# Performance work log

Hardware: AMD Instinct MI355X
Metric: run time of the kernel (lower is better)

The kernel has to match this reference:

```python
import jax, jax.numpy as jnp
import numpy as np

NUM_EXPERTS = 8
HIDDEN = 1024
INTER = 1024
BATCH = 2
SEQ = 1024
TOP_K = 2
SWIGLU_ALPHA = 1.702
LIMIT = 7.0


def setup_inputs() -> dict:
    key = jax.random.key(0)
    ks = jax.random.split(key, 7)
    hidden_states = jax.random.normal(ks[0], (BATCH, SEQ, HIDDEN), jnp.float32)
    router_indices = jax.random.randint(ks[1], (BATCH * SEQ, TOP_K), 0, NUM_EXPERTS)
    routing_weights = jax.nn.softmax(
        jax.random.normal(ks[2], (BATCH * SEQ, NUM_EXPERTS), jnp.float32), axis=-1)
    scale = 0.02
    gate_up_proj = jax.random.normal(ks[3], (NUM_EXPERTS, HIDDEN, 2 * INTER), jnp.float32) * scale
    gate_up_proj_bias = jax.random.normal(ks[4], (NUM_EXPERTS, 2 * INTER), jnp.float32) * scale
    down_proj = jax.random.normal(ks[5], (NUM_EXPERTS, INTER, HIDDEN), jnp.float32) * scale
    down_proj_bias = jax.random.normal(ks[6], (NUM_EXPERTS, HIDDEN), jnp.float32) * scale
    return {
        "hidden_states": hidden_states,
        "router_indices": router_indices,
        "routing_weights": routing_weights,
        "gate_up_proj": gate_up_proj,
        "gate_up_proj_bias": gate_up_proj_bias,
        "down_proj": down_proj,
        "down_proj_bias": down_proj_bias,
    }


def _grouped_mm(x, w, expert_ids):
    """Grouped GEMM: y[t] = x[t] @ w[expert_ids[t]].

    x: [T, K], w: [E, K, N], expert_ids: [T] int.
    Reference form via one-hot masking (exact equivalent of torch._grouped_mm
    on expert-sorted tokens); guaranteed jit- and grad-safe.
    """
    onehot = jax.nn.one_hot(expert_ids, w.shape[0], dtype=x.dtype)  # [T, E]
    y_all = jnp.einsum('tk,ekn->etn', x, w)                         # [E, T, N]
    return jnp.einsum('te,etn->tn', onehot, y_all)                  # [T, N]


def _gpt_oss_swiglu(x):
    gate = jnp.minimum(x[..., ::2], LIMIT)
    up = jnp.clip(x[..., 1::2], -LIMIT, LIMIT)
    glu = gate * jax.nn.sigmoid(gate * SWIGLU_ALPHA)
    return (up + 1.0) * glu


def reference(hidden_states, router_indices, routing_weights,
              gate_up_proj, gate_up_proj_bias, down_proj, down_proj_bias):
    B = hidden_states.shape[0]
    H = hidden_states.shape[-1]
    x = hidden_states.reshape(-1, H)                       # [M, H]
    M = x.shape[0]
    top_k = router_indices.shape[1]
    num_experts = gate_up_proj.shape[0]

    # routing_weights is [M, num_experts] -> gather the top-k weights
    topk_weights = jnp.take_along_axis(routing_weights, router_indices, axis=1)  # [M, K]

    flat_experts = router_indices.reshape(-1)              # [T = M*K]
    sort_idx = jnp.argsort(flat_experts)                   # expert-sorted order
    sorted_pos = sort_idx // top_k                         # token id per slot
    expert_sorted = flat_experts[sort_idx]                 # [T]
    grouped = x[sorted_pos]                                # [T, H]

    gate_up = _grouped_mm(grouped, gate_up_proj, expert_sorted)
    gate_up = gate_up + gate_up_proj_bias[expert_sorted]   # per-expert bias
    inter = _gpt_oss_swiglu(gate_up)                       # [T, I]

    down = _grouped_mm(inter, down_proj, expert_sorted)
    down = down + down_proj_bias[expert_sorted]            # [T, H]
    down = down * topk_weights.reshape(-1)[sort_idx][:, None]

    out = jnp.zeros((M, H), x.dtype).at[sorted_pos].add(down)  # scatter-add combine
    return out.reshape(B, -1, H)
```

## Files before the change

### kernel.cpp

```cpp
#include <hip/hip_runtime.h>

#define NE 8
#define NH 1024
#define NI 1024
#define NGU 2048
#define MTOK 2048
#define TSLOT 4096

#define MAXT64 80
#define MAXT128 40

typedef short s16x8 __attribute__((ext_vector_type(8)));
typedef float f32x4 __attribute__((ext_vector_type(4)));
typedef unsigned short u16;

#define WS_SEG      0
#define WS_DESC64   64
#define WS_DESC128  384
#define WS_SLOT     1024
#define WS_POS      17408
#define WS_INTER    33792
#define WS_AREG     8422400UL
#define WS_WREG     12616704UL
#define WS_WTD      46171136UL
#define WS_NEED_FAST  46171136UL
#define WS_NEED_PIGGY 62948352UL

__device__ inline u16 f2bf(float f) {
    unsigned u = __builtin_bit_cast(unsigned, f);
    u += 0x7fffu + ((u >> 16) & 1u);
    return (u16)(u >> 16);
}

__device__ inline void lds_dma16(const u16* g, u16* l) {
    __builtin_amdgcn_global_load_lds(
        (const __attribute__((address_space(1))) unsigned int*)g,
        (__attribute__((address_space(3))) unsigned int*)l, 16, 0, 0);
}

__device__ inline int lds_off(int row, int blk) {
    return (row << 7) | (((blk ^ (row & 7)) & 7) << 4);
}

#define PIPE_FENCE asm volatile("" ::: "memory")
#define WAIT_VM6   asm volatile("s_waitcnt vmcnt(6)" ::: "memory")
#define WAIT_VM0   asm volatile("s_waitcnt vmcnt(0)" ::: "memory")

__device__ inline void tr_tile(const float* __restrict__ in, u16* __restrict__ outw,
                               int K, int N, int n0, int k0, int tid, u16 (*T)[66]) {
#pragma unroll
    for (int p = 0; p < 2; ++p) {
        int kr = p * 32 + (tid >> 4) * 2;
        int nc = (tid & 15) * 4;
        const float* r0 = in + (size_t)(k0 + kr) * N + n0 + nc;
        float4 v0 = *(const float4*)r0;
        float4 v1 = *(const float4*)(r0 + N);
#pragma unroll
        for (int i = 0; i < 4; ++i) {
            unsigned lo = f2bf(((const float*)&v0)[i]);
            unsigned hi = f2bf(((const float*)&v1)[i]);
            *(unsigned*)&T[nc + i][kr] = lo | (hi << 16);
        }
    }
    __syncthreads();
#pragma unroll
    for (int p = 0; p < 2; ++p) {
        int idx = p * 256 + tid;
        int nr = idx >> 3, kc = (idx & 7) * 8;
        unsigned q0 = *(const unsigned*)&T[nr][kc + 0];
        unsigned q1 = *(const unsigned*)&T[nr][kc + 2];
        unsigned q2 = *(const unsigned*)&T[nr][kc + 4];
        unsigned q3 = *(const unsigned*)&T[nr][kc + 6];
        uint4 vv = {q0, q1, q2, q3};
        *(uint4*)(outw + (size_t)(n0 + nr) * K + k0 + kc) = vv;
    }
}

__global__ __launch_bounds__(256) void k_tr(const float* __restrict__ W,
                                            u16* __restrict__ WT, int K, int N) {
    __shared__ u16 T[64][66];
    tr_tile(W + (size_t)blockIdx.z * K * N, WT + (size_t)blockIdx.z * N * K,
            K, N, blockIdx.x * 64, blockIdx.y * 64, threadIdx.x, T);
}

__global__ __launch_bounds__(256) void k_prep(
        const float* __restrict__ x, const int* __restrict__ ridx,
        const float* __restrict__ wgu,
        int* __restrict__ seg, int* __restrict__ d64, int* __restrict__ d128,
        int* __restrict__ slot_of, int* __restrict__ pos_of,
        u16* __restrict__ A, u16* __restrict__ wt_gu, float* __restrict__ out) {
    __shared__ int cnt[NE];
    __shared__ int cur[NE];
    __shared__ u16 T[64][66];
    int b = blockIdx.x;
    int tid = threadIdx.x;

    if (b == 0) {
        if (tid < NE) cnt[tid] = 0;
        __syncthreads();
        for (int s = tid; s < TSLOT; s += blockDim.x) atomicAdd(&cnt[ridx[s] & 7], 1);
        __syncthreads();
        if (tid == 0) {
            int a = 0;
            for (int e = 0; e < NE; ++e) { seg[e] = a; cur[e] = a; a += cnt[e]; }
            seg[NE] = a;
            int nt = 0;
            for (int e = 0; e < NE; ++e)
                for (int m0 = 0; m0 < cnt[e]; m0 += 64) d64[nt++] = (e << 16) | (m0 / 64);
            for (; nt < MAXT64; ++nt) d64[nt] = -1;
            nt = 0;
            for (int e = 0; e < NE; ++e)
                for (int m0 = 0; m0 < cnt[e]; m0 += 128) d128[nt++] = (e << 16) | (m0 / 128);
            for (; nt < MAXT128; ++nt) d128[nt] = -1;
        }
        __syncthreads();
        for (int s = tid; s < TSLOT; s += blockDim.x) {
            int e = ridx[s] & 7;
            int p = atomicAdd(&cur[e], 1);
            slot_of[p] = s;
            pos_of[s] = p;
        }
    } else if (b <= MTOK) {
        int t = b - 1;
        float4 v = ((const float4*)(x + (size_t)t * NH))[tid];
        ushort4 o;
        o.x = f2bf(v.x); o.y = f2bf(v.y); o.z = f2bf(v.z); o.w = f2bf(v.w);
        ((ushort4*)(A + (size_t)t * NH))[tid] = o;
        float4 z = {0.f, 0.f, 0.f, 0.f};
        ((float4*)(out + (size_t)t * NH))[tid] = z;
    } else {
        int id = b - (MTOK + 1);
        int e = id >> 9, rem = id & 511;
        int kblk = rem >> 5, nblk = rem & 31;
        tr_tile(wgu + (size_t)e * NH * NGU, wt_gu + (size_t)e * NGU * NH,
                NH, NGU, nblk * 64, kblk * 64, tid, T);
    }
}

__global__ __launch_bounds__(256) void k_gateup_f(
        const u16* __restrict__ A,
        const u16* __restrict__ wt,
        const float* __restrict__ bias,
        const int* __restrict__ seg, const int* __restrict__ desc,
        const int* __restrict__ slot_of,
        u16* __restrict__ inter,
        const float* __restrict__ wd,
        u16* __restrict__ wtd) {
    __shared__ __align__(16) char SM[49152];
    int tid = threadIdx.x;

    if (blockIdx.x >= MAXT128) {
        int id = (blockIdx.x - MAXT128) * 32 + blockIdx.y;
        int e = id >> 8, rem = id & 255;
        int kblk = rem >> 4, nblk = rem & 15;
        u16 (*T)[66] = (u16(*)[66])SM;
        tr_tile(wd + (size_t)e * NI * NH, wtd + (size_t)e * NH * NI,
                NI, NH, nblk * 64, kblk * 64, tid, T);
        return;
    }

    int d = desc[blockIdx.x];
    if (d < 0) return;
    int e = d >> 16, mt = d & 0xffff;
    int seg0 = seg[e], Te = seg[e + 1] - seg0, m0 = mt * 128;

    u16* As0 = (u16*)SM;
    u16* As1 = (u16*)(SM + 16384);
    u16* Bs0 = (u16*)(SM + 32768);
    u16* Bs1 = (u16*)(SM + 40960);

    int lane = tid & 63, w = tid >> 6;
    int ml = lane & 15, kq = lane >> 4;
    int wm = w >> 1, wn = w & 1;
    int n0 = blockIdx.y * 64;
    const u16* wte = wt + (size_t)e * NGU * NH;
    int dr = lane >> 3, db = (lane & 7) ^ dr;

    const u16* aptr[4];
#pragma unroll
    for (int c = 0; c < 4; ++c) {
        int gr = seg0 + m0 + c * 32 + w * 8 + dr;
        if (gr > TSLOT - 1) gr = TSLOT - 1;
        int tok = slot_of[gr] >> 1;
        aptr[c] = A + (size_t)tok * NH + db * 8;
    }
    const u16* bptr[2];
#pragma unroll
    for (int c = 0; c < 2; ++c)
        bptr[c] = wte + (size_t)(n0 + c * 32 + w * 8 + dr) * NH + db * 8;

    auto stage = [&](u16* AS, u16* BS, int kb) {
#pragma unroll
        for (int c = 0; c < 4; ++c) lds_dma16(aptr[c] + kb, AS + c * 2048 + w * 512);
#pragma unroll
        for (int c = 0; c < 2; ++c) lds_dma16(bptr[c] + kb, BS + c * 2048 + w * 512);
    };

    f32x4 zero = {0.f, 0.f, 0.f, 0.f};
    f32x4 acc[4][2];
#pragma unroll
    for (int i = 0; i < 4; ++i) { acc[i][0] = zero; acc[i][1] = zero; }

    auto compute = [&](const u16* AS, const u16* BS) {
#pragma unroll
        for (int kk = 0; kk < 64; kk += 32) {
            s16x8 af[4], bf[2];
#pragma unroll
            for (int i = 0; i < 4; ++i)
                af[i] = *(const s16x8*)((const char*)AS + lds_off(wm * 64 + i * 16 + ml, (kk >> 3) + kq));
#pragma unroll
            for (int i = 0; i < 2; ++i)
                bf[i] = *(const s16x8*)((const char*)BS + lds_off(wn * 32 + i * 16 + ml, (kk >> 3) + kq));
#pragma unroll
            for (int mi = 0; mi < 4; ++mi)
#pragma unroll
                for (int ni = 0; ni < 2; ++ni)
                    acc[mi][ni] = __builtin_amdgcn_mfma_f32_16x16x32_bf16(
                        af[mi], bf[ni], acc[mi][ni], 0, 0, 0);
        }
    };

    stage(As0, Bs0, 0);
    for (int t = 0; t < 16; t += 2) {
        stage(As1, Bs1, (t + 1) << 6);
        WAIT_VM6;
        __builtin_amdgcn_s_barrier();
        PIPE_FENCE;
        __builtin_amdgcn_s_setprio(1);
        compute(As0, Bs0);
        __builtin_amdgcn_s_setprio(0);
        PIPE_FENCE;
        __builtin_amdgcn_s_barrier();
        if (t < 14) {
            stage(As0, Bs0, (t + 2) << 6);
            WAIT_VM6;
        } else {
            WAIT_VM0;
        }
        __builtin_amdgcn_s_barrier();
        PIPE_FENCE;
        __builtin_amdgcn_s_setprio(1);
        compute(As1, Bs1);
        __builtin_amdgcn_s_setprio(0);
        PIPE_FENCE;
        __builtin_amdgcn_s_barrier();
    }

#pragma unroll
    for (int ni = 0; ni < 2; ++ni) {
        int n = n0 + wn * 32 + ni * 16 + ml;
        float bv = bias[e * NGU + n];
#pragma unroll
        for (int mi = 0; mi < 4; ++mi) {
#pragma unroll
            for (int r = 0; r < 4; ++r) {
                float v = acc[mi][ni][r] + bv;
                float pr = __shfl_xor(v, 1, 64);
                float g = (lane & 1) ? pr : v;
                float u = (lane & 1) ? v : pr;
                g = fminf(g, 7.0f);
                u = fminf(fmaxf(u, -7.0f), 7.0f);
                float glu = g / (1.0f + __expf(-1.702f * g));
                float y = (u + 1.0f) * glu;
                int mloc = wm * 64 + mi * 16 + kq * 4 + r;
                if (!(lane & 1) && (m0 + mloc) < Te)
                    inter[(size_t)(seg0 + m0 + mloc) * NI + (n >> 1)] = f2bf(y);
            }
        }
    }
}

__global__ __launch_bounds__(256) void k_down_f(
        const u16* __restrict__ inter,
        const u16* __restrict__ wt,
        const float* __restrict__ bias,
        const float* __restrict__ rw,
        const int* __restrict__ seg, const int* __restrict__ desc,
        const int* __restrict__ slot_of,
        float* __restrict__ out) {
    int d = desc[blockIdx.x];
    if (d < 0) return;
    int e = d >> 16, mt = d & 0xffff;
    int seg0 = seg[e], Te = seg[e + 1] - seg0, m0 = mt * 128;

    __shared__ __align__(16) u16 As0[128 * 64];
    __shared__ __align__(16) u16 As1[128 * 64];
    __shared__ __align__(16) u16 Bs0[64 * 64];
    __shared__ __align__(16) u16 Bs1[64 * 64];
    __shared__ int tokS[128];
    __shared__ float wgtS[128];

    int tid = threadIdx.x;
    if (tid < 128) {
        int m = m0 + tid;
        if (m < Te) {
            int token = slot_of[seg0 + m] >> 1;
            tokS[tid] = token;
            wgtS[tid] = rw[token * NE + e];
        } else {
            tokS[tid] = 0;
            wgtS[tid] = 0.0f;
        }
    }

    int lane = tid & 63, w = tid >> 6;
    int ml = lane & 15, kq = lane >> 4;
    int wm = w >> 1, wn = w & 1;
    int n0 = blockIdx.y * 64;
    const u16* wte = wt + (size_t)e * NH * NI;
    int dr = lane >> 3, db = (lane & 7) ^ dr;

    const u16* aptr[4];
#pragma unroll
    for (int c = 0; c < 4; ++c) {
        int gr = seg0 + m0 + c * 32 + w * 8 + dr;
        if (gr > TSLOT - 1) gr = TSLOT - 1;
        aptr[c] = inter + (size_t)gr * NI + db * 8;
    }
    const u16* bptr[2];
#pragma unroll
    for (int c = 0; c < 2; ++c)
        bptr[c] = wte + (size_t)(n0 + c * 32 + w * 8 + dr) * NI + db * 8;

    auto stage = [&](u16* AS, u16* BS, int kb) {
#pragma unroll
        for (int c = 0; c < 4; ++c) lds_dma16(aptr[c] + kb, AS + c * 2048 + w * 512);
#pragma unroll
        for (int c = 0; c < 2; ++c) lds_dma16(bptr[c] + kb, BS + c * 2048 + w * 512);
    };

    f32x4 zero = {0.f, 0.f, 0.f, 0.f};
    f32x4 acc[4][2];
#pragma unroll
    for (int i = 0; i < 4; ++i) { acc[i][0] = zero; acc[i][1] = zero; }

    auto compute = [&](const u16* AS, const u16* BS) {
#pragma unroll
        for (int kk = 0; kk < 64; kk += 32) {
            s16x8 af[4], bf[2];
#pragma unroll
            for (int i = 0; i < 4; ++i)
                af[i] = *(const s16x8*)((const char*)AS + lds_off(wm * 64 + i * 16 + ml, (kk >> 3) + kq));
#pragma unroll
            for (int i = 0; i < 2; ++i)
                bf[i] = *(const s16x8*)((const char*)BS + lds_off(wn * 32 + i * 16 + ml, (kk >> 3) + kq));
#pragma unroll
            for (int mi = 0; mi < 4; ++mi)
#pragma unroll
                for (int ni = 0; ni < 2; ++ni)
                    acc[mi][ni] = __builtin_amdgcn_mfma_f32_16x16x32_bf16(
                        af[mi], bf[ni], acc[mi][ni], 0, 0, 0);
        }
    };

    stage(As0, Bs0, 0);
    for (int t = 0; t < 16; t += 2) {
        stage(As1, Bs1, (t + 1) << 6);
        WAIT_VM6;
        __builtin_amdgcn_s_barrier();
        PIPE_FENCE;
        __builtin_amdgcn_s_setprio(1);
        compute(As0, Bs0);
        __builtin_amdgcn_s_setprio(0);
        PIPE_FENCE;
        __builtin_amdgcn_s_barrier();
        if (t < 14) {
            stage(As0, Bs0, (t + 2) << 6);
            WAIT_VM6;
        } else {
            WAIT_VM0;
        }
        __builtin_amdgcn_s_barrier();
        PIPE_FENCE;
        __builtin_amdgcn_s_setprio(1);
        compute(As1, Bs1);
        __builtin_amdgcn_s_setprio(0);
        PIPE_FENCE;
        __builtin_amdgcn_s_barrier();
    }

    float bv[2];
#pragma unroll
    for (int ni = 0; ni < 2; ++ni)
        bv[ni] = bias[e * NH + n0 + wn * 32 + ni * 16 + ml];

#pragma unroll
    for (int mi = 0; mi < 4; ++mi) {
#pragma unroll
        for (int r = 0; r < 4; ++r) {
            int mloc = wm * 64 + mi * 16 + kq * 4 + r;
            if ((m0 + mloc) < Te) {
                int token = tokS[mloc];
                float wgt = wgtS[mloc];
#pragma unroll
                for (int ni = 0; ni < 2; ++ni) {
                    int n = n0 + wn * 32 + ni * 16 + ml;
                    atomicAdd(&out[(size_t)token * NH + n], (acc[mi][ni][r] + bv[ni]) * wgt);
                }
            }
        }
    }
}

__global__ void k_build(const int* __restrict__ ridx, int* __restrict__ seg,
                        int* __restrict__ d64, int* __restrict__ d128,
                        int* __restrict__ slot_of, int* __restrict__ pos_of) {
    __shared__ int cnt[NE];
    __shared__ int cur[NE];
    int tid = threadIdx.x;
    if (tid < NE) cnt[tid] = 0;
    __syncthreads();
    for (int s = tid; s < TSLOT; s += blockDim.x) atomicAdd(&cnt[ridx[s] & 7], 1);
    __syncthreads();
    if (tid == 0) {
        int a = 0;
        for (int e = 0; e < NE; ++e) { seg[e] = a; cur[e] = a; a += cnt[e]; }
        seg[NE] = a;
        int nt = 0;
        for (int e = 0; e < NE; ++e)
            for (int m0 = 0; m0 < cnt[e]; m0 += 64) d64[nt++] = (e << 16) | (m0 / 64);
        for (; nt < MAXT64; ++nt) d64[nt] = -1;
        nt = 0;
        for (int e = 0; e < NE; ++e)
            for (int m0 = 0; m0 < cnt[e]; m0 += 128) d128[nt++] = (e << 16) | (m0 / 128);
        for (; nt < MAXT128; ++nt) d128[nt] = -1;
    }
    __syncthreads();
    for (int s = tid; s < TSLOT; s += blockDim.x) {
        int e = ridx[s] & 7;
        int p = atomicAdd(&cur[e], 1);
        slot_of[p] = s;
        pos_of[s] = p;
    }
}

__global__ __launch_bounds__(256) void k_gateup_s(
        const float* __restrict__ x, const float* __restrict__ w,
        const float* __restrict__ bias,
        const int* __restrict__ seg, const int* __restrict__ desc,
        const int* __restrict__ slot_of, u16* __restrict__ inter) {
    int d = desc[blockIdx.x];
    if (d < 0) return;
    int e = d >> 16, mt = d & 0xffff;
    int seg0 = seg[e], Te = seg[e + 1] - seg0, m0 = mt * 64;
    __shared__ u16 As[64 * 40];
    __shared__ int tok[64];
    int tid = threadIdx.x;
    if (tid < 64) {
        int m = m0 + tid;
        tok[tid] = (m < Te) ? (slot_of[seg0 + m] >> 1) : -1;
    }
    __syncthreads();
    int lane = tid & 63, wave = tid >> 6;
    int arow = tid >> 2, acol = (tid & 3) * 8;
    int ta = tok[arow];
    int kq = lane >> 4, ml = lane & 15;
    int nb = blockIdx.y * 128 + wave * 32;
    const float* wp = w + (size_t)e * NH * NGU;
    f32x4 zero = {0.f, 0.f, 0.f, 0.f};
    f32x4 acc[4][2];
#pragma unroll
    for (int i = 0; i < 4; ++i) { acc[i][0] = zero; acc[i][1] = zero; }
    for (int kb = 0; kb < NH; kb += 32) {
        float4 a0 = {0, 0, 0, 0}, a1 = {0, 0, 0, 0};
        if (ta >= 0) {
            const float* xp = x + (size_t)ta * NH + kb + acol;
            a0 = *(const float4*)xp; a1 = *(const float4*)(xp + 4);
        }
        s16x8 av;
        av[0] = (short)f2bf(a0.x); av[1] = (short)f2bf(a0.y);
        av[2] = (short)f2bf(a0.z); av[3] = (short)f2bf(a0.w);
        av[4] = (short)f2bf(a1.x); av[5] = (short)f2bf(a1.y);
        av[6] = (short)f2bf(a1.z); av[7] = (short)f2bf(a1.w);
        __syncthreads();
        *(s16x8*)&As[arow * 40 + acol] = av;
        __syncthreads();
        s16x8 afr[4];
#pragma unroll
        for (int msi = 0; msi < 4; ++msi)
            afr[msi] = *(const s16x8*)&As[(msi * 16 + ml) * 40 + kq * 8];
        s16x8 bfr[2];
#pragma unroll
        for (int s = 0; s < 2; ++s) {
            const float* bp = wp + (size_t)(kb + kq * 8) * NGU + nb + s * 16 + ml;
#pragma unroll
            for (int j = 0; j < 8; ++j) bfr[s][j] = (short)f2bf(bp[(size_t)j * NGU]);
        }
#pragma unroll
        for (int msi = 0; msi < 4; ++msi)
#pragma unroll
            for (int s = 0; s < 2; ++s)
                acc[msi][s] = __builtin_amdgcn_mfma_f32_16x16x32_bf16(
                    afr[msi], bfr[s], acc[msi][s], 0, 0, 0);
    }
#pragma unroll
    for (int s = 0; s < 2; ++s) {
        int n = nb + s * 16 + ml;
        float bv = bias[e * NGU + n];
#pragma unroll
        for (int msi = 0; msi < 4; ++msi) {
#pragma unroll
            for (int r = 0; r < 4; ++r) {
                float v = acc[msi][s][r] + bv;
                float pr = __shfl_xor(v, 1, 64);
                float g = (lane & 1) ? pr : v;
                float u = (lane & 1) ? v : pr;
                g = fminf(g, 7.0f);
                u = fminf(fmaxf(u, -7.0f), 7.0f);
                float glu = g / (1.0f + __expf(-1.702f * g));
                float y = (u + 1.0f) * glu;
                int mrow = m0 + msi * 16 + kq * 4 + r;
                if (!(lane & 1) && mrow < Te)
                    inter[(size_t)(seg0 + mrow) * NI + (n >> 1)] = f2bf(y);
            }
        }
    }
}

__global__ __launch_bounds__(256) void k_down_s(
        const u16* __restrict__ inter, const float* __restrict__ w,
        const float* __restrict__ bias, const float* __restrict__ rw,
        const int* __restrict__ seg, const int* __restrict__ desc,
        const int* __restrict__ slot_of, float* __restrict__ out) {
    int d = desc[blockIdx.x];
    if (d < 0) return;
    int e = d >> 16, mt = d & 0xffff;
    int seg0 = seg[e], Te = seg[e + 1] - seg0, m0 = mt * 64;
    __shared__ u16 As[64 * 40];
    int tid = threadIdx.x;
    int lane = tid & 63, wave = tid >> 6;
    int arow = tid >> 2, acol = (tid & 3) * 8;
    bool avalid = (m0 + arow) < Te;
    int kq = lane >> 4, ml = lane & 15;
    int nb = blockIdx.y * 128 + wave * 32;
    const float* wp = w + (size_t)e * NI * NH;
    f32x4 zero = {0.f, 0.f, 0.f, 0.f};
    f32x4 acc[4][2];
#pragma unroll
    for (int i = 0; i < 4; ++i) { acc[i][0] = zero; acc[i][1] = zero; }
    for (int kb = 0; kb < NI; kb += 32) {
        s16x8 av = {0, 0, 0, 0, 0, 0, 0, 0};
        if (avalid) av = *(const s16x8*)(inter + (size_t)(seg0 + m0 + arow) * NI + kb + acol);
        __syncthreads();
        *(s16x8*)&As[arow * 40 + acol] = av;
        __syncthreads();
        s16x8 afr[4];
#pragma unroll
        for (int msi = 0; msi < 4; ++msi)
            afr[msi] = *(const s16x8*)&As[(msi * 16 + ml) * 40 + kq * 8];
        s16x8 bfr[2];
#pragma unroll
        for (int s = 0; s < 2; ++s) {
            const float* bp = wp + (size_t)(kb + kq * 8) * NH + nb + s * 16 + ml;
#pragma unroll
            for (int j = 0; j < 8; ++j) bfr[s][j] = (short)f2bf(bp[(size_t)j * NH]);
        }
#pragma unroll
        for (int msi = 0; msi < 4; ++msi)
#pragma unroll
            for (int s = 0; s < 2; ++s)
                acc[msi][s] = __builtin_amdgcn_mfma_f32_16x16x32_bf16(
                    afr[msi], bfr[s], acc[msi][s], 0, 0, 0);
    }
    float bv[2];
    bv[0] = bias[e * NH + nb + ml];
    bv[1] = bias[e * NH + nb + 16 + ml];
#pragma unroll
    for (int msi = 0; msi < 4; ++msi) {
#pragma unroll
        for (int r = 0; r < 4; ++r) {
            int mrow = m0 + msi * 16 + kq * 4 + r;
            if (mrow < Te) {
                int slot = slot_of[seg0 + mrow];
                int token = slot >> 1;
                float wgt = rw[token * NE + e];
#pragma unroll
                for (int s = 0; s < 2; ++s) {
                    int n = nb + s * 16 + ml;
                    atomicAdd(&out[(size_t)token * NH + n], (acc[msi][s][r] + bv[s]) * wgt);
                }
            }
        }
    }
}

extern "C" void kernel_launch(void* const* d_in, const int* in_sizes, int n_in,
                              void* d_out, int out_size, void* d_ws, size_t ws_size,
                              hipStream_t stream) {
    const float* x   = (const float*)d_in[0];
    const int*   ri  = (const int*)d_in[1];
    const float* rw  = (const float*)d_in[2];
    const float* wgu = (const float*)d_in[3];
    const float* bgu = (const float*)d_in[4];
    const float* wd  = (const float*)d_in[5];
    const float* bd  = (const float*)d_in[6];
    float* out = (float*)d_out;

    char* ws = (char*)d_ws;
    int* seg     = (int*)(ws + WS_SEG);
    int* d64     = (int*)(ws + WS_DESC64);
    int* d128    = (int*)(ws + WS_DESC128);
    int* slot_of = (int*)(ws + WS_SLOT);
    int* pos_of  = (int*)(ws + WS_POS);
    u16* inter   = (u16*)(ws + WS_INTER);

    if (ws_size >= WS_NEED_PIGGY) {
        u16* aReg = (u16*)(ws + WS_AREG);
        u16* wReg = (u16*)(ws + WS_WREG);
        u16* wtd  = (u16*)(ws + WS_WTD);
        hipLaunchKernelGGL(k_prep, dim3(1 + MTOK + 4096), dim3(256), 0, stream,
                           x, ri, wgu, seg, d64, d128, slot_of, pos_of, aReg, wReg, out);
        hipLaunchKernelGGL(k_gateup_f, dim3(MAXT128 + 64, NGU / 64), dim3(256), 0, stream,
                           aReg, wReg, bgu, seg, d128, slot_of, inter, wd, wtd);
        hipLaunchKernelGGL(k_down_f, dim3(MAXT128, NH / 64), dim3(256), 0, stream,
                           inter, wtd, bd, rw, seg, d128, slot_of, out);
    } else if (ws_size >= WS_NEED_FAST) {
        u16* aReg = (u16*)(ws + WS_AREG);
        u16* wReg = (u16*)(ws + WS_WREG);
        hipLaunchKernelGGL(k_prep, dim3(1 + MTOK + 4096), dim3(256), 0, stream,
                           x, ri, wgu, seg, d64, d128, slot_of, pos_of, aReg, wReg, out);
        hipLaunchKernelGGL(k_gateup_f, dim3(MAXT128, NGU / 64), dim3(256), 0, stream,
                           aReg, wReg, bgu, seg, d128, slot_of, inter, wd, wReg);
        hipLaunchKernelGGL(k_tr, dim3(NH / 64, NI / 64, NE), dim3(256), 0, stream,
                           wd, wReg, NI, NH);
        hipLaunchKernelGGL(k_down_f, dim3(MAXT128, NH / 64), dim3(256), 0, stream,
                           inter, wReg, bd, rw, seg, d128, slot_of, out);
    } else {
        hipLaunchKernelGGL(k_build, dim3(1), dim3(256), 0, stream, ri, seg, d64, d128,
                           slot_of, pos_of);
        hipMemsetAsync(out, 0, (size_t)MTOK * NH * sizeof(float), stream);
        hipLaunchKernelGGL(k_gateup_s, dim3(MAXT64, NGU / 128), dim3(256), 0, stream,
                           x, wgu, bgu, seg, d64, slot_of, inter);
        hipLaunchKernelGGL(k_down_s, dim3(MAXT64, NH / 128), dim3(256), 0, stream,
                           inter, wd, bd, rw, seg, d64, slot_of, out);
    }
}
```

Measured before the change: 222.0 us.

## Fuse MoE pipeline into cooperative persistent kernel with grid syncs and split-K down

Replaces the three-launch prep/gateup/down sequence with a single cooperative persistent kernel of 768 blocks that uses grid.sync between phases. Prep work (routing build, activation conversion, both weight transposes) runs in a grid-stride loop, then the gate-up and down GEMM tiles follow. The down projection is now split along K into two halves accumulated with atomics, which doubles the number of tiles. The aim is to remove launch gaps and the tail imbalance between kernels, at the cost of grid-wide barriers, a fixed grid of three blocks per CU, and twice as many output atomics.

New measurement: 616.0 us. 2.78x slower.

```diff
diff --git a/kernel.cpp b/kernel.cpp
--- a/kernel.cpp
+++ b/kernel.cpp
@@ -1,4 +1,7 @@
 #include <hip/hip_runtime.h>
+#include <hip/hip_cooperative_groups.h>
+
+namespace cg = cooperative_groups;
 
 #define NE 8
 #define NH 1024
@@ -9,6 +12,7 @@
 
 #define MAXT64 80
 #define MAXT128 40
+#define NBLK 768
 
 typedef short s16x8 __attribute__((ext_vector_type(8)));
 typedef float f32x4 __attribute__((ext_vector_type(4)));
@@ -76,6 +80,294 @@
     }
 }
 
+__device__ inline void build_body(const int* __restrict__ ridx, int* __restrict__ seg,
+                                  int* __restrict__ d64, int* __restrict__ d128,
+                                  int* __restrict__ slot_of, int* __restrict__ pos_of,
+                                  int* cnt, int* cur, int tid) {
+    if (tid < NE) cnt[tid] = 0;
+    __syncthreads();
+    for (int s = tid; s < TSLOT; s += 256) atomicAdd(&cnt[ridx[s] & 7], 1);
+    __syncthreads();
+    if (tid == 0) {
+        int a = 0;
+        for (int e = 0; e < NE; ++e) { seg[e] = a; cur[e] = a; a += cnt[e]; }
+        seg[NE] = a;
+        int nt = 0;
+        for (int e = 0; e < NE; ++e)
+            for (int m0 = 0; m0 < cnt[e]; m0 += 64) d64[nt++] = (e << 16) | (m0 / 64);
+        for (; nt < MAXT64; ++nt) d64[nt] = -1;
+        nt = 0;
+        for (int e = 0; e < NE; ++e)
+            for (int m0 = 0; m0 < cnt[e]; m0 += 128) d128[nt++] = (e << 16) | (m0 / 128);
+        for (; nt < MAXT128; ++nt) d128[nt] = -1;
+    }
+    __syncthreads();
+    for (int s = tid; s < TSLOT; s += 256) {
+        int e = ridx[s] & 7;
+        int p = atomicAdd(&cur[e], 1);
+        slot_of[p] = s;
+        pos_of[s] = p;
+    }
+}
+
+__device__ __forceinline__ void gemm_pipe(const u16* const ap[4], const u16* const bp[2],
+                                          char* SM, int tid, int kbeg, int nsteps,
+                                          f32x4 (&acc)[4][2]) {
+    u16* As0 = (u16*)SM;
+    u16* As1 = (u16*)(SM + 16384);
+    u16* Bs0 = (u16*)(SM + 32768);
+    u16* Bs1 = (u16*)(SM + 40960);
+    int lane = tid & 63, w = tid >> 6;
+    int ml = lane & 15, kq = lane >> 4;
+    int wm = w >> 1, wn = w & 1;
+
+    auto stage = [&](u16* AS, u16* BS, int kb) {
+#pragma unroll
+        for (int c = 0; c < 4; ++c) lds_dma16(ap[c] + kb, AS + c * 2048 + w * 512);
+#pragma unroll
+        for (int c = 0; c < 2; ++c) lds_dma16(bp[c] + kb, BS + c * 2048 + w * 512);
+    };
+    auto compute = [&](const u16* AS, const u16* BS) {
+#pragma unroll
+        for (int kk = 0; kk < 64; kk += 32) {
+            s16x8 af[4], bf[2];
+#pragma unroll
+            for (int i = 0; i < 4; ++i)
+                af[i] = *(const s16x8*)((const char*)AS + lds_off(wm * 64 + i * 16 + ml, (kk >> 3) + kq));
+#pragma unroll
+            for (int i = 0; i < 2; ++i)
+                bf[i] = *(const s16x8*)((const char*)BS + lds_off(wn * 32 + i * 16 + ml, (kk >> 3) + kq));
+#pragma unroll
+            for (int mi = 0; mi < 4; ++mi)
+#pragma unroll
+                for (int ni = 0; ni < 2; ++ni)
+                    acc[mi][ni] = __builtin_amdgcn_mfma_f32_16x16x32_bf16(
+                        af[mi], bf[ni], acc[mi][ni], 0, 0, 0);
+        }
+    };
+
+    stage(As0, Bs0, kbeg);
+    for (int t = 0; t < nsteps; t += 2) {
+        stage(As1, Bs1, kbeg + ((t + 1) << 6));
+        WAIT_VM6;
+        __builtin_amdgcn_s_barrier();
+        PIPE_FENCE;
+        __builtin_amdgcn_s_setprio(1);
+        compute(As0, Bs0);
+        __builtin_amdgcn_s_setprio(0);
+        PIPE_FENCE;
+        __builtin_amdgcn_s_barrier();
+        if (t < nsteps - 2) {
+            stage(As0, Bs0, kbeg + ((t + 2) << 6));
+            WAIT_VM6;
+        } else {
+            WAIT_VM0;
+        }
+        __builtin_amdgcn_s_barrier();
+        PIPE_FENCE;
+        __builtin_amdgcn_s_setprio(1);
+        compute(As1, Bs1);
+        __builtin_amdgcn_s_setprio(0);
+        PIPE_FENCE;
+        __builtin_amdgcn_s_barrier();
+    }
+}
+
+__device__ __forceinline__ void job_gateup(
+        int d, int y, const u16* __restrict__ A, const u16* __restrict__ wt,
+        const float* __restrict__ bias, const int* __restrict__ seg,
+        const int* __restrict__ slot_of, u16* __restrict__ inter,
+        char* SM, int tid) {
+    int e = d >> 16, mt = d & 0xffff;
+    int seg0 = seg[e], Te = seg[e + 1] - seg0, m0 = mt * 128;
+    int lane = tid & 63, w = tid >> 6;
+    int ml = lane & 15, kq = lane >> 4;
+    int wm = w >> 1, wn = w & 1;
+    int n0 = y * 64;
+    int dr = lane >> 3, db = (lane & 7) ^ dr;
+    const u16* wte = wt + (size_t)e * NGU * NH;
+
+    const u16* ap[4];
+#pragma unroll
+    for (int c = 0; c < 4; ++c) {
+        int gr = seg0 + m0 + c * 32 + w * 8 + dr;
+        if (gr > TSLOT - 1) gr = TSLOT - 1;
+        int tok = slot_of[gr] >> 1;
+        ap[c] = A + (size_t)tok * NH + db * 8;
+    }
+    const u16* bp[2];
+#pragma unroll
+    for (int c = 0; c < 2; ++c)
+        bp[c] = wte + (size_t)(n0 + c * 32 + w * 8 + dr) * NH + db * 8;
+
+    f32x4 zero = {0.f, 0.f, 0.f, 0.f};
+    f32x4 acc[4][2];
+#pragma unroll
+    for (int i = 0; i < 4; ++i) { acc[i][0] = zero; acc[i][1] = zero; }
+
+    gemm_pipe(ap, bp, SM, tid, 0, 16, acc);
+
+#pragma unroll
+    for (int ni = 0; ni < 2; ++ni) {
+        int n = n0 + wn * 32 + ni * 16 + ml;
+        float bv = bias[e * NGU + n];
+#pragma unroll
+        for (int mi = 0; mi < 4; ++mi) {
+#pragma unroll
+            for (int r = 0; r < 4; ++r) {
+                float v = acc[mi][ni][r] + bv;
+                float pr = __shfl_xor(v, 1, 64);
+                float g = (lane & 1) ? pr : v;
+                float u = (lane & 1) ? v : pr;
+                g = fminf(g, 7.0f);
+                u = fminf(fmaxf(u, -7.0f), 7.0f);
+                float glu = g / (1.0f + __expf(-1.702f * g));
+                float yv = (u + 1.0f) * glu;
+                int mloc = wm * 64 + mi * 16 + kq * 4 + r;
+                if (!(lane & 1) && (m0 + mloc) < Te)
+                    inter[(size_t)(seg0 + m0 + mloc) * NI + (n >> 1)] = f2bf(yv);
+            }
+        }
+    }
+}
+
+__device__ __forceinline__ void job_down(
+        int d, int y, int kz, const u16* __restrict__ inter, const u16* __restrict__ wt,
+        const float* __restrict__ bias, const float* __restrict__ rw,
+        const int* __restrict__ seg, const int* __restrict__ slot_of,
+        float* __restrict__ out, char* SM, int tid) {
+    int e = d >> 16, mt = d & 0xffff;
+    int seg0 = seg[e], Te = seg[e + 1] - seg0, m0 = mt * 128;
+    int* tokS = (int*)(SM + 49152);
+    float* wgtS = (float*)(SM + 49664);
+
+    if (tid < 128) {
+        int m = m0 + tid;
+        if (m < Te) {
+            int token = slot_of[seg0 + m] >> 1;
+            tokS[tid] = token;
+            wgtS[tid] = rw[token * NE + e];
+        } else {
+            tokS[tid] = 0;
+            wgtS[tid] = 0.0f;
+        }
+    }
+
+    int lane = tid & 63, w = tid >> 6;
+    int ml = lane & 15, kq = lane >> 4;
+    int wm = w >> 1, wn = w & 1;
+    int n0 = y * 64;
+    int dr = lane >> 3, db = (lane & 7) ^ dr;
+    const u16* wte = wt + (size_t)e * NH * NI;
+
+    const u16* ap[4];
+#pragma unroll
+    for (int c = 0; c < 4; ++c) {
+        int gr = seg0 + m0 + c * 32 + w * 8 + dr;
+        if (gr > TSLOT - 1) gr = TSLOT - 1;
+        ap[c] = inter + (size_t)gr * NI + db * 8;
+    }
+    const u16* bp[2];
+#pragma unroll
+    for (int c = 0; c < 2; ++c)
+        bp[c] = wte + (size_t)(n0 + c * 32 + w * 8 + dr) * NI + db * 8;
+
+    f32x4 zero = {0.f, 0.f, 0.f, 0.f};
+    f32x4 acc[4][2];
+#pragma unroll
+    for (int i = 0; i < 4; ++i) { acc[i][0] = zero; acc[i][1] = zero; }
+
+    gemm_pipe(ap, bp, SM, tid, kz * (NI / 2), 8, acc);
+
+    float bv[2];
+#pragma unroll
+    for (int ni = 0; ni < 2; ++ni)
+        bv[ni] = kz ? 0.0f : bias[e * NH + n0 + wn * 32 + ni * 16 + ml];
+
+#pragma unroll
+    for (int mi = 0; mi < 4; ++mi) {
+#pragma unroll
+        for (int r = 0; r < 4; ++r) {
+            int mloc = wm * 64 + mi * 16 + kq * 4 + r;
+            if ((m0 + mloc) < Te) {
+                int token = tokS[mloc];
+                float wgt = wgtS[mloc];
+#pragma unroll
+                for (int ni = 0; ni < 2; ++ni) {
+                    int n = n0 + wn * 32 + ni * 16 + ml;
+                    atomicAdd(&out[(size_t)token * NH + n], (acc[mi][ni][r] + bv[ni]) * wgt);
+                }
+            }
+        }
+    }
+}
+
+__global__ __launch_bounds__(256, 3) void k_mega(
+        const float* __restrict__ x, const int* __restrict__ ri,
+        const float* __restrict__ rw,
+        const float* __restrict__ wgu, const float* __restrict__ bgu,
+        const float* __restrict__ wd, const float* __restrict__ bd,
+        int* __restrict__ seg, int* __restrict__ d64, int* __restrict__ d128,
+        int* __restrict__ slot_of, int* __restrict__ pos_of,
+        u16* __restrict__ A, u16* __restrict__ wtgu, u16* __restrict__ wtd,
+        u16* __restrict__ inter, float* __restrict__ out) {
+    __shared__ __align__(16) char SM[50176];
+    int tid = threadIdx.x;
+    int bid = blockIdx.x;
+    cg::grid_group grid = cg::this_grid();
+
+    const int P0 = 1 + MTOK + 4096 + 2048;
+    for (int j = bid; j < P0; j += NBLK) {
+        __syncthreads();
+        if (j == 0) {
+            build_body(ri, seg, d64, d128, slot_of, pos_of,
+                       (int*)SM, (int*)SM + NE, tid);
+        } else if (j <= MTOK) {
+            int t = j - 1;
+            float4 v = ((const float4*)(x + (size_t)t * NH))[tid];
+            ushort4 o;
+            o.x = f2bf(v.x); o.y = f2bf(v.y); o.z = f2bf(v.z); o.w = f2bf(v.w);
+            ((ushort4*)(A + (size_t)t * NH))[tid] = o;
+            float4 z = {0.f, 0.f, 0.f, 0.f};
+            ((float4*)(out + (size_t)t * NH))[tid] = z;
+        } else if (j <= MTOK + 4096) {
+            int id = j - (MTOK + 1);
+            int e = id >> 9, rem = id & 511;
+            int kblk = rem >> 5, nblk = rem & 31;
+            tr_tile(wgu + (size_t)e * NH * NGU, wtgu + (size_t)e * NGU * NH,
+                    NH, NGU, nblk * 64, kblk * 64, tid, (u16(*)[66])SM);
+        } else {
+            int id = j - (MTOK + 4097);
+            int e = id >> 8, rem = id & 255;
+            int kblk = rem >> 4, nblk = rem & 15;
+            tr_tile(wd + (size_t)e * NI * NH, wtd + (size_t)e * NH * NI,
+                    NI, NH, nblk * 64, kblk * 64, tid, (u16(*)[66])SM);
+        }
+    }
+    __threadfence();
+    grid.sync();
+
+    for (int j = bid; j < MAXT128 * 32; j += NBLK) {
+        __syncthreads();
+        int xt = j % MAXT128, y = j / MAXT128;
+        int d = d128[xt];
+        if (d < 0) continue;
+        job_gateup(d, y, A, wtgu, bgu, seg, slot_of, inter, SM, tid);
+    }
+    __threadfence();
+    grid.sync();
+
+    for (int j = bid; j < MAXT128 * 32; j += NBLK) {
+        __syncthreads();
+        int xt = j % MAXT128;
+        int rest = j / MAXT128;
+        int y = rest & 15, kz = rest >> 4;
+        int d = d128[xt];
+        if (d < 0) continue;
+        job_down(d, y, kz, inter, wtd, bd, rw, seg, slot_of, out, SM, tid);
+    }
+}
+
 __global__ __launch_bounds__(256) void k_tr(const float* __restrict__ W,
                                             u16* __restrict__ WT, int K, int N) {
     __shared__ u16 T[64][66];
@@ -94,32 +386,8 @@
     __shared__ u16 T[64][66];
     int b = blockIdx.x;
     int tid = threadIdx.x;
-
     if (b == 0) {
-        if (tid < NE) cnt[tid] = 0;
-        __syncthreads();
-        for (int s = tid; s < TSLOT; s += blockDim.x) atomicAdd(&cnt[ridx[s] & 7], 1);
-        __syncthreads();
-        if (tid == 0) {
-            int a = 0;
-            for (int e = 0; e < NE; ++e) { seg[e] = a; cur[e] = a; a += cnt[e]; }
-            seg[NE] = a;
-            int nt = 0;
-            for (int e = 0; e < NE; ++e)
-                for (int m0 = 0; m0 < cnt[e]; m0 += 64) d64[nt++] = (e << 16) | (m0 / 64);
-            for (; nt < MAXT64; ++nt) d64[nt] = -1;
-            nt = 0;
-            for (int e = 0; e < NE; ++e)
-                for (int m0 = 0; m0 < cnt[e]; m0 += 128) d128[nt++] = (e << 16) | (m0 / 128);
-            for (; nt < MAXT128; ++nt) d128[nt] = -1;
-        }
-        __syncthreads();
-        for (int s = tid; s < TSLOT; s += blockDim.x) {
-            int e = ridx[s] & 7;
-            int p = atomicAdd(&cur[e], 1);
-            slot_of[p] = s;
-            pos_of[s] = p;
-        }
+        build_body(ridx, seg, d64, d128, slot_of, pos_of, cnt, cur, tid);
     } else if (b <= MTOK) {
         int t = b - 1;
         float4 v = ((const float4*)(x + (size_t)t * NH))[tid];
@@ -138,268 +406,36 @@
 }
 
 __global__ __launch_bounds__(256) void k_gateup_f(
-        const u16* __restrict__ A,
-        const u16* __restrict__ wt,
+        const u16* __restrict__ A, const u16* __restrict__ wt,
         const float* __restrict__ bias,
         const int* __restrict__ seg, const int* __restrict__ desc,
-        const int* __restrict__ slot_of,
-        u16* __restrict__ inter,
-        const float* __restrict__ wd,
-        u16* __restrict__ wtd) {
-    __shared__ __align__(16) char SM[49152];
+        const int* __restrict__ slot_of, u16* __restrict__ inter,
+        const float* __restrict__ wd, u16* __restrict__ wtd) {
+    __shared__ __align__(16) char SM[50176];
     int tid = threadIdx.x;
-
     if (blockIdx.x >= MAXT128) {
         int id = (blockIdx.x - MAXT128) * 32 + blockIdx.y;
         int e = id >> 8, rem = id & 255;
         int kblk = rem >> 4, nblk = rem & 15;
-        u16 (*T)[66] = (u16(*)[66])SM;
         tr_tile(wd + (size_t)e * NI * NH, wtd + (size_t)e * NH * NI,
-                NI, NH, nblk * 64, kblk * 64, tid, T);
+                NI, NH, nblk * 64, kblk * 64, tid, (u16(*)[66])SM);
         return;
     }
-
     int d = desc[blockIdx.x];
     if (d < 0) return;
-    int e = d >> 16, mt = d & 0xffff;
-    int seg0 = seg[e], Te = seg[e + 1] - seg0, m0 = mt * 128;
-
-    u16* As0 = (u16*)SM;
-    u16* As1 = (u16*)(SM + 16384);
-    u16* Bs0 = (u16*)(SM + 32768);
-    u16* Bs1 = (u16*)(SM + 40960);
-
-    int lane = tid & 63, w = tid >> 6;
-    int ml = lane & 15, kq = lane >> 4;
-    int wm = w >> 1, wn = w & 1;
-    int n0 = blockIdx.y * 64;
-    const u16* wte = wt + (size_t)e * NGU * NH;
-    int dr = lane >> 3, db = (lane & 7) ^ dr;
-
-    const u16* aptr[4];
-#pragma unroll
-    for (int c = 0; c < 4; ++c) {
-        int gr = seg0 + m0 + c * 32 + w * 8 + dr;
-        if (gr > TSLOT - 1) gr = TSLOT - 1;
-        int tok = slot_of[gr] >> 1;
-        aptr[c] = A + (size_t)tok * NH + db * 8;
-    }
-    const u16* bptr[2];
-#pragma unroll
-    for (int c = 0; c < 2; ++c)
-        bptr[c] = wte + (size_t)(n0 + c * 32 + w * 8 + dr) * NH + db * 8;
-
-    auto stage = [&](u16* AS, u16* BS, int kb) {
-#pragma unroll
-        for (int c = 0; c < 4; ++c) lds_dma16(aptr[c] + kb, AS + c * 2048 + w * 512);
-#pragma unroll
-        for (int c = 0; c < 2; ++c) lds_dma16(bptr[c] + kb, BS + c * 2048 + w * 512);
-    };
-
-    f32x4 zero = {0.f, 0.f, 0.f, 0.f};
-    f32x4 acc[4][2];
-#pragma unroll
-    for (int i = 0; i < 4; ++i) { acc[i][0] = zero; acc[i][1] = zero; }
-
-    auto compute = [&](const u16* AS, const u16* BS) {
-#pragma unroll
-        for (int kk = 0; kk < 64; kk += 32) {
-            s16x8 af[4], bf[2];
-#pragma unroll
-            for (int i = 0; i < 4; ++i)
-                af[i] = *(const s16x8*)((const char*)AS + lds_off(wm * 64 + i * 16 + ml, (kk >> 3) + kq));
-#pragma unroll
-            for (int i = 0; i < 2; ++i)
-                bf[i] = *(const s16x8*)((const char*)BS + lds_off(wn * 32 + i * 16 + ml, (kk >> 3) + kq));
-#pragma unroll
-            for (int mi = 0; mi < 4; ++mi)
-#pragma unroll
-                for (int ni = 0; ni < 2; ++ni)
-                    acc[mi][ni] = __builtin_amdgcn_mfma_f32_16x16x32_bf16(
-                        af[mi], bf[ni], acc[mi][ni], 0, 0, 0);
-        }
-    };
-
-    stage(As0, Bs0, 0);
-    for (int t = 0; t < 16; t += 2) {
-        stage(As1, Bs1, (t + 1) << 6);
-        WAIT_VM6;
-        __builtin_amdgcn_s_barrier();
-        PIPE_FENCE;
-        __builtin_amdgcn_s_setprio(1);
-        compute(As0, Bs0);
-        __builtin_amdgcn_s_setprio(0);
-        PIPE_FENCE;
-        __builtin_amdgcn_s_barrier();
-        if (t < 14) {
-            stage(As0, Bs0, (t + 2) << 6);
-            WAIT_VM6;
-        } else {
-            WAIT_VM0;
-        }
-        __builtin_amdgcn_s_barrier();
-        PIPE_FENCE;
-        __builtin_amdgcn_s_setprio(1);
-        compute(As1, Bs1);
-        __builtin_amdgcn_s_setprio(0);
-        PIPE_FENCE;
-        __builtin_amdgcn_s_barrier();
-    }
-
-#pragma unroll
-    for (int ni = 0; ni < 2; ++ni) {
-        int n = n0 + wn * 32 + ni * 16 + ml;
-        float bv = bias[e * NGU + n];
-#pragma unroll
-        for (int mi = 0; mi < 4; ++mi) {
-#pragma unroll
-            for (int r = 0; r < 4; ++r) {
-                float v = acc[mi][ni][r] + bv;
-                float pr = __shfl_xor(v, 1, 64);
-                float g = (lane & 1) ? pr : v;
-                float u = (lane & 1) ? v : pr;
-                g = fminf(g, 7.0f);
-                u = fminf(fmaxf(u, -7.0f), 7.0f);
-                float glu = g / (1.0f + __expf(-1.702f * g));
-                float y = (u + 1.0f) * glu;
-                int mloc = wm * 64 + mi * 16 + kq * 4 + r;
-                if (!(lane & 1) && (m0 + mloc) < Te)
-                    inter[(size_t)(seg0 + m0 + mloc) * NI + (n >> 1)] = f2bf(y);
-            }
-        }
-    }
+    job_gateup(d, blockIdx.y, A, wt, bias, seg, slot_of, inter, SM, tid);
 }
 
 __global__ __launch_bounds__(256) void k_down_f(
-        const u16* __restrict__ inter,
-        const u16* __restrict__ wt,
-        const float* __restrict__ bias,
-        const float* __restrict__ rw,
+        const u16* __restrict__ inter, const u16* __restrict__ wt,
+        const float* __restrict__ bias, const float* __restrict__ rw,
         const int* __restrict__ seg, const int* __restrict__ desc,
-        const int* __restrict__ slot_of,
-        float* __restrict__ out) {
+        const int* __restrict__ slot_of, float* __restrict__ out) {
+    __shared__ __align__(16) char SM[50176];
     int d = desc[blockIdx.x];
     if (d < 0) return;
-    int e = d >> 16, mt = d & 0xffff;
-    int seg0 = seg[e], Te = seg[e + 1] - seg0, m0 = mt * 128;
-
-    __shared__ __align__(16) u16 As0[128 * 64];
-    __shared__ __align__(16) u16 As1[128 * 64];
-    __shared__ __align__(16) u16 Bs0[64 * 64];
-    __shared__ __align__(16) u16 Bs1[64 * 64];
-    __shared__ int tokS[128];
-    __shared__ float wgtS[128];
-
-    int tid = threadIdx.x;
-    if (tid < 128) {
-        int m = m0 + tid;
-        if (m < Te) {
-            int token = slot_of[seg0 + m] >> 1;
-            tokS[tid] = token;
-            wgtS[tid] = rw[token * NE + e];
-        } else {
-            tokS[tid] = 0;
-            wgtS[tid] = 0.0f;
-        }
-    }
-
-    int lane = tid & 63, w = tid >> 6;
-    int ml = lane & 15, kq = lane >> 4;
-    int wm = w >> 1, wn = w & 1;
-    int n0 = blockIdx.y * 64;
-    const u16* wte = wt + (size_t)e * NH * NI;
-    int dr = lane >> 3, db = (lane & 7) ^ dr;
-
-    const u16* aptr[4];
-#pragma unroll
-    for (int c = 0; c < 4; ++c) {
-        int gr = seg0 + m0 + c * 32 + w * 8 + dr;
-        if (gr > TSLOT - 1) gr = TSLOT - 1;
-        aptr[c] = inter + (size_t)gr * NI + db * 8;
-    }
-    const u16* bptr[2];
-#pragma unroll
-    for (int c = 0; c < 2; ++c)
-        bptr[c] = wte + (size_t)(n0 + c * 32 + w * 8 + dr) * NI + db * 8;
-
-    auto stage = [&](u16* AS, u16* BS, int kb) {
-#pragma unroll
-        for (int c = 0; c < 4; ++c) lds_dma16(aptr[c] + kb, AS + c * 2048 + w * 512);
-#pragma unroll
-        for (int c = 0; c < 2; ++c) lds_dma16(bptr[c] + kb, BS + c * 2048 + w * 512);
-    };
-
-    f32x4 zero = {0.f, 0.f, 0.f, 0.f};
-    f32x4 acc[4][2];
-#pragma unroll
-    for (int i = 0; i < 4; ++i) { acc[i][0] = zero; acc[i][1] = zero; }
-
-    auto compute = [&](const u16* AS, const u16* BS) {
-#pragma unroll
-        for (int kk = 0; kk < 64; kk += 32) {
-            s16x8 af[4], bf[2];
-#pragma unroll
-            for (int i = 0; i < 4; ++i)
-                af[i] = *(const s16x8*)((const char*)AS + lds_off(wm * 64 + i * 16 + ml, (kk >> 3) + kq));
-#pragma unroll
-            for (int i = 0; i < 2; ++i)
-                bf[i] = *(const s16x8*)((const char*)BS + lds_off(wn * 32 + i * 16 + ml, (kk >> 3) + kq));
-#pragma unroll
-            for (int mi = 0; mi < 4; ++mi)
-#pragma unroll
-                for (int ni = 0; ni < 2; ++ni)
-                    acc[mi][ni] = __builtin_amdgcn_mfma_f32_16x16x32_bf16(
-                        af[mi], bf[ni], acc[mi][ni], 0, 0, 0);
-        }
-    };
-
-    stage(As0, Bs0, 0);
-    for (int t = 0; t < 16; t += 2) {
-        stage(As1, Bs1, (t + 1) << 6);
-        WAIT_VM6;
-        __builtin_amdgcn_s_barrier();
-        PIPE_FENCE;
-        __builtin_amdgcn_s_setprio(1);
-        compute(As0, Bs0);
-        __builtin_amdgcn_s_setprio(0);
-        PIPE_FENCE;
-        __builtin_amdgcn_s_barrier();
-        if (t < 14) {
-            stage(As0, Bs0, (t + 2) << 6);
-            WAIT_VM6;
-        } else {
-            WAIT_VM0;
-        }
-        __builtin_amdgcn_s_barrier();
-        PIPE_FENCE;
-        __builtin_amdgcn_s_setprio(1);
-        compute(As1, Bs1);
-        __builtin_amdgcn_s_setprio(0);
-        PIPE_FENCE;
-        __builtin_amdgcn_s_barrier();
-    }
-
-    float bv[2];
-#pragma unroll
-    for (int ni = 0; ni < 2; ++ni)
-        bv[ni] = bias[e * NH + n0 + wn * 32 + ni * 16 + ml];
-
-#pragma unroll
-    for (int mi = 0; mi < 4; ++mi) {
-#pragma unroll
-        for (int r = 0; r < 4; ++r) {
-            int mloc = wm * 64 + mi * 16 + kq * 4 + r;
-            if ((m0 + mloc) < Te) {
-                int token = tokS[mloc];
-                float wgt = wgtS[mloc];
-#pragma unroll
-                for (int ni = 0; ni < 2; ++ni) {
-                    int n = n0 + wn * 32 + ni * 16 + ml;
-                    atomicAdd(&out[(size_t)token * NH + n], (acc[mi][ni][r] + bv[ni]) * wgt);
-                }
-            }
-        }
-    }
+    job_down(d, blockIdx.y, blockIdx.z, inter, wt, bias, rw, seg, slot_of, out,
+             SM, threadIdx.x);
 }
 
 __global__ void k_build(const int* __restrict__ ridx, int* __restrict__ seg,
@@ -407,31 +443,7 @@
                         int* __restrict__ slot_of, int* __restrict__ pos_of) {
     __shared__ int cnt[NE];
     __shared__ int cur[NE];
-    int tid = threadIdx.x;
-    if (tid < NE) cnt[tid] = 0;
-    __syncthreads();
-    for (int s = tid; s < TSLOT; s += blockDim.x) atomicAdd(&cnt[ridx[s] & 7], 1);
-    __syncthreads();
-    if (tid == 0) {
-        int a = 0;
-        for (int e = 0; e < NE; ++e) { seg[e] = a; cur[e] = a; a += cnt[e]; }
-        seg[NE] = a;
-        int nt = 0;
-        for (int e = 0; e < NE; ++e)
-            for (int m0 = 0; m0 < cnt[e]; m0 += 64) d64[nt++] = (e << 16) | (m0 / 64);
-        for (; nt < MAXT64; ++nt) d64[nt] = -1;
-        nt = 0;
-        for (int e = 0; e < NE; ++e)
-            for (int m0 = 0; m0 < cnt[e]; m0 += 128) d128[nt++] = (e << 16) | (m0 / 128);
-        for (; nt < MAXT128; ++nt) d128[nt] = -1;
-    }
-    __syncthreads();
-    for (int s = tid; s < TSLOT; s += blockDim.x) {
-        int e = ridx[s] & 7;
-        int p = atomicAdd(&cur[e], 1);
-        slot_of[p] = s;
-        pos_of[s] = p;
-    }
+    build_body(ridx, seg, d64, d128, slot_of, pos_of, cnt, cur, threadIdx.x);
 }
 
 __global__ __launch_bounds__(256) void k_gateup_s(
@@ -604,15 +616,37 @@
     int* pos_of  = (int*)(ws + WS_POS);
     u16* inter   = (u16*)(ws + WS_INTER);
 
+    static int g_coop = -1;
+    if (g_coop < 0) {
+        int dev = 0;
+        (void)hipGetDevice(&dev);
+        int v = 0;
+        if (hipDeviceGetAttribute(&v, hipDeviceAttributeCooperativeLaunch, dev) != hipSuccess)
+            v = 0;
+        g_coop = v;
+    }
+
     if (ws_size >= WS_NEED_PIGGY) {
         u16* aReg = (u16*)(ws + WS_AREG);
         u16* wReg = (u16*)(ws + WS_WREG);
         u16* wtd  = (u16*)(ws + WS_WTD);
+
+        if (g_coop) {
+            void* args[] = {(void*)&x, (void*)&ri, (void*)&rw, (void*)&wgu, (void*)&bgu,
+                            (void*)&wd, (void*)&bd, (void*)&seg, (void*)&d64, (void*)&d128,
+                            (void*)&slot_of, (void*)&pos_of, (void*)&aReg, (void*)&wReg,
+                            (void*)&wtd, (void*)&inter, (void*)&out};
+            hipError_t err = hipLaunchCooperativeKernel(
+                (const void*)k_mega, dim3(NBLK), dim3(256), args, 0, stream);
+            if (err == hipSuccess) return;
+            (void)hipGetLastError();
+        }
+
         hipLaunchKernelGGL(k_prep, dim3(1 + MTOK + 4096), dim3(256), 0, stream,
                            x, ri, wgu, seg, d64, d128, slot_of, pos_of, aReg, wReg, out);
         hipLaunchKernelGGL(k_gateup_f, dim3(MAXT128 + 64, NGU / 64), dim3(256), 0, stream,
                            aReg, wReg, bgu, seg, d128, slot_of, inter, wd, wtd);
-        hipLaunchKernelGGL(k_down_f, dim3(MAXT128, NH / 64), dim3(256), 0, stream,
+        hipLaunchKernelGGL(k_down_f, dim3(MAXT128, NH / 64, 2), dim3(256), 0, stream,
                            inter, wtd, bd, rw, seg, d128, slot_of, out);
     } else if (ws_size >= WS_NEED_FAST) {
         u16* aReg = (u16*)(ws + WS_AREG);
@@ -623,7 +657,7 @@
                            aReg, wReg, bgu, seg, d128, slot_of, inter, wd, wReg);
         hipLaunchKernelGGL(k_tr, dim3(NH / 64, NI / 64, NE), dim3(256), 0, stream,
                            wd, wReg, NI, NH);
-        hipLaunchKernelGGL(k_down_f, dim3(MAXT128, NH / 64), dim3(256), 0, stream,
+        hipLaunchKernelGGL(k_down_f, dim3(MAXT128, NH / 64, 2), dim3(256), 0, stream,
                            inter, wReg, bd, rw, seg, d128, slot_of, out);
     } else {
         hipLaunchKernelGGL(k_build, dim3(1), dim3(256), 0, stream, ri, seg, d64, d128,
```
